# Kernel tuning notes

Hardware: AMD Instinct MI355X
Metric: run time of the kernel (lower is better)

The kernel has to match this reference:

```python
import jax, jax.numpy as jnp
import numpy as np

N_HEAD = 16
D_MODEL = 1024
D_K = 64
D_V = 64
TEMPER = float(np.power(D_MODEL, 0.5))  # NOTE: source scales by sqrt(d_model), not sqrt(d_k)


def setup_inputs() -> dict:
    key = jax.random.key(0)
    ks = jax.random.split(key, 6)
    B, T = 4, 2048
    q = jax.random.normal(ks[0], (B, T, D_MODEL), dtype=jnp.float32)
    k = jax.random.normal(ks[1], (B, T, D_MODEL), dtype=jnp.float32)
    v = jax.random.normal(ks[2], (B, T, D_MODEL), dtype=jnp.float32)
    # xavier_normal for [out, in] = [n_head*d, d_model]; stored as [d_model, n_head*d] for x @ W
    def xavier(kk, fan_out, fan_in):
        std = float(np.sqrt(2.0 / (fan_in + fan_out)))
        return jax.random.normal(kk, (fan_in, fan_out), dtype=jnp.float32) * std
    W_Q = xavier(ks[3], N_HEAD * D_K, D_MODEL)
    W_K = xavier(ks[4], N_HEAD * D_K, D_MODEL)
    W_V = xavier(ks[5], N_HEAD * D_V, D_MODEL)
    return {"q": q, "k": k, "v": v, "W_Q": W_Q, "W_K": W_K, "W_V": W_V}


def reference(q, k, v, W_Q, W_K, W_V):
    B, Tq, _ = q.shape
    Tk = k.shape[1]
    residual = q
    # project and split heads: [B, T, H, d]
    qh = (q @ W_Q).reshape(B, Tq, N_HEAD, D_K)
    kh = (k @ W_K).reshape(B, Tk, N_HEAD, D_K)
    vh = (v @ W_V).reshape(B, Tk, N_HEAD, D_V)
    # scaled dot-product attention (dropout is identity in eval)
    attn = jnp.einsum('bqhd,bkhd->bhqk', qh, kh) / TEMPER
    attn = jax.nn.softmax(attn, axis=-1)
    out = jnp.einsum('bhqk,bkhd->bqhd', attn, vh).reshape(B, Tq, N_HEAD * D_V)
    return out + residual
```

## Files before the change

kernel.cpp:

```cpp
#include <hip/hip_runtime.h>
#include <cstdint>
#include <cstddef>

typedef __bf16 bf16x8 __attribute__((ext_vector_type(8)));
typedef float f32x4 __attribute__((ext_vector_type(4)));
typedef unsigned short u16;
typedef unsigned int u32;

static constexpr int T = 2048;
static constexpr int DM = 1024;
static constexpr float QSCALE = 0.04508422f;

#define GLOBAL_AS __attribute__((address_space(1)))
#define LDS_AS __attribute__((address_space(3)))

__device__ __forceinline__ void gld_lds16(const u16* g, u16* l) {
  __builtin_amdgcn_global_load_lds((const GLOBAL_AS u32*)g, (LDS_AS u32*)l, 16, 0, 0);
}

__device__ __forceinline__ u16 f2bf(float f) {
  u32 u = __builtin_bit_cast(u32, f);
  u += 0x7fffu + ((u >> 16) & 1u);
  return (u16)(u >> 16);
}

__device__ __forceinline__ u32 pkb(float lo, float hi) {
#if __has_builtin(__builtin_amdgcn_cvt_pk_bf16_f32)
  typedef __bf16 bf16x2 __attribute__((ext_vector_type(2)));
  bf16x2 r = __builtin_amdgcn_cvt_pk_bf16_f32(lo, hi);
  return __builtin_bit_cast(u32, r);
#else
  return __builtin_amdgcn_perm(__builtin_bit_cast(u32, hi),
                               __builtin_bit_cast(u32, lo), 0x07060302u);
#endif
}

__device__ __forceinline__ float fexp2(float x) {
#if __has_builtin(__builtin_amdgcn_exp2f)
  return __builtin_amdgcn_exp2f(x);
#else
  return __builtin_exp2f(x);
#endif
}

__device__ __forceinline__ void pl16swap(u32& a, u32& b) {
  asm("v_permlane16_swap_b32 %0, %1" : "+v"(a), "+v"(b));
}
__device__ __forceinline__ void pl32swap(u32& a, u32& b) {
  asm("v_permlane32_swap_b32 %0, %1" : "+v"(a), "+v"(b));
}

__global__ __launch_bounds__(256) void xcvt(
    const float* __restrict__ q, const float* __restrict__ k, const float* __restrict__ v,
    u16* __restrict__ oq, u16* __restrict__ ok, u16* __restrict__ ov) {
  const float* X = blockIdx.y == 0 ? q : blockIdx.y == 1 ? k : v;
  u16* O = blockIdx.y == 0 ? oq : blockIdx.y == 1 ? ok : ov;
  const size_t i = ((size_t)blockIdx.x * 256 + threadIdx.x) * 8;
  float4 a0 = *(const float4*)(X + i), a1 = *(const float4*)(X + i + 4);
  uint4 p;
  p.x = pkb(a0.x, a0.y); p.y = pkb(a0.z, a0.w);
  p.z = pkb(a1.x, a1.y); p.w = pkb(a1.z, a1.w);
  *(uint4*)(O + i) = p;
}

__global__ __launch_bounds__(256) void wt_kernel(
    const float* __restrict__ W0, const float* __restrict__ W1, const float* __restrict__ W2,
    u16* __restrict__ O0, u16* __restrict__ O1, u16* __restrict__ O2) {
  const float* W = blockIdx.z == 0 ? W0 : blockIdx.z == 1 ? W1 : W2;
  u16* O = blockIdx.z == 0 ? O0 : blockIdx.z == 1 ? O1 : O2;
  const float sc = blockIdx.z == 0 ? QSCALE : 1.0f;
  const int k0 = blockIdx.x * 64, n0 = blockIdx.y * 64;
  __shared__ float tile[64][68];
  const int tid = threadIdx.x;
#pragma unroll
  for (int it = 0; it < 4; ++it) {
    int chunk = tid + it * 256;
    int r = chunk >> 4, c4 = (chunk & 15) * 4;
    *(float4*)&tile[r][c4] = *(const float4*)(W + (size_t)(k0 + r) * DM + n0 + c4);
  }
  __syncthreads();
#pragma unroll
  for (int it = 0; it < 4; ++it) {
    int chunk = tid + it * 256;
    int n = chunk >> 4, k4 = (chunk & 15) * 4;
    ushort4 o;
    o.x = f2bf(tile[k4 + 0][n] * sc);
    o.y = f2bf(tile[k4 + 1][n] * sc);
    o.z = f2bf(tile[k4 + 2][n] * sc);
    o.w = f2bf(tile[k4 + 3][n] * sc);
    *(ushort4*)(O + (size_t)(n0 + n) * DM + k0 + k4) = o;
  }
}

__global__ __launch_bounds__(256, 3) void gemm_proj(
    const u16* __restrict__ Xq, const u16* __restrict__ Xk, const u16* __restrict__ Xv,
    const u16* __restrict__ Wq, const u16* __restrict__ Wk, const u16* __restrict__ Wv,
    u16* __restrict__ Oq, u16* __restrict__ Ok, u16* __restrict__ VHt) {
  const int z = blockIdx.y;
  const u16* X = z == 0 ? Xq : z == 1 ? Xk : Xv;
  const u16* Wt = z == 0 ? Wq : z == 1 ? Wk : Wv;
  const int xcd = blockIdx.x & 7, j = blockIdx.x >> 3;
  const int n0 = (j & 7) * 128;
  const int m0 = (xcd * 8 + (j >> 3)) * 128;
  __shared__ u16 Al[128][64];
  __shared__ u16 Bl[128][64];
  const int tid = threadIdx.x, w = tid >> 6, lane = tid & 63;
  const int c16 = lane & 15, quad = lane >> 4;
  const int wm = (w >> 1) * 64, wn = (w & 1) * 64;
  const int rk = lane >> 3;
  const int ck = ((lane & 7) ^ rk) * 8;
  const int swz = c16 & 7;
  f32x4 acc[4][4] = {};
  const u16* ga = X + (size_t)(m0 + w * 32 + rk) * DM + ck;
  const u16* gb = Wt + (size_t)(n0 + w * 32 + rk) * DM + ck;
  for (int kk = 0; kk < 1024; kk += 64) {
    __syncthreads();
#pragma unroll
    for (int i = 0; i < 4; ++i) {
      gld_lds16(ga + kk + (size_t)(i * 8) * DM, &Al[w * 32 + i * 8][0]);
      gld_lds16(gb + kk + (size_t)(i * 8) * DM, &Bl[w * 32 + i * 8][0]);
    }
    __syncthreads();
#pragma unroll
    for (int s = 0; s < 2; ++s) {
      bf16x8 af[4], bfr[4];
#pragma unroll
      for (int t = 0; t < 4; ++t) af[t] = *(const bf16x8*)&Al[wm + t * 16 + c16][((quad + 4 * s) ^ swz) * 8];
#pragma unroll
      for (int t = 0; t < 4; ++t) bfr[t] = *(const bf16x8*)&Bl[wn + t * 16 + c16][((quad + 4 * s) ^ swz) * 8];
#pragma unroll
      for (int mt = 0; mt < 4; ++mt)
#pragma unroll
        for (int nt = 0; nt < 4; ++nt)
          acc[mt][nt] = __builtin_amdgcn_mfma_f32_16x16x32_bf16(af[mt], bfr[nt], acc[mt][nt], 0, 0, 0);
    }
  }
  if (z < 2) {
    u16* O = z == 0 ? Oq : Ok;
#pragma unroll
    for (int mt = 0; mt < 4; ++mt)
#pragma unroll
      for (int nt = 0; nt < 4; ++nt)
#pragma unroll
        for (int r = 0; r < 4; ++r) {
          size_t row = m0 + wm + mt * 16 + quad * 4 + r;
          size_t col = n0 + wn + nt * 16 + c16;
          O[row * DM + col] = f2bf(acc[mt][nt][r]);
        }
  } else {
#pragma unroll
    for (int mt = 0; mt < 4; ++mt)
#pragma unroll
      for (int nt = 0; nt < 4; ++nt) {
        const int row0 = m0 + wm + mt * 16 + quad * 4;
        const int col = n0 + wn + nt * 16 + c16;
        const int bb = row0 >> 11, t0 = row0 & 2047;
        const int hh = col >> 6, dd = col & 63;
        ushort4 o;
        o.x = f2bf(acc[mt][nt][0]);
        o.y = f2bf(acc[mt][nt][1]);
        o.z = f2bf(acc[mt][nt][2]);
        o.w = f2bf(acc[mt][nt][3]);
        *(ushort4*)(VHt + ((size_t)((bb * 16 + hh) * 64 + dd)) * T + t0) = o;
      }
  }
}

__global__ __launch_bounds__(256, 4) void flash_kernel(
    const u16* __restrict__ QH, const u16* __restrict__ KH, const u16* __restrict__ VHt,
    const float* __restrict__ res, float* __restrict__ out) {
  const int blk = blockIdx.x;
  const int x = blk & 7, g = blk >> 3;
  const int bh = x * 8 + (g & 7);
  const int qb = g >> 3;
  const int b = bh >> 4, h = bh & 15;
  const int tid = threadIdx.x, w = tid >> 6, lane = tid & 63;
  const int c16 = lane & 15, quad = lane >> 4;
  const int swzq = c16 & 7;
  __shared__ u16 Kl[2][64][64];
  __shared__ u16 Vt[2][64][64];
  __shared__ float Ll[4][2][16];
  const int qbase = qb * 128 + w * 32;
  bf16x8 bq[2][2];
#pragma unroll
  for (int qi = 0; qi < 2; ++qi) {
    const u16* qp = QH + (size_t)(b * T + qbase + qi * 16 + c16) * DM + h * 64 + quad * 8;
    bq[qi][0] = *(const bf16x8*)qp;
    bq[qi][1] = *(const bf16x8*)(qp + 32);
  }
  f32x4 acc[2][4] = {};
  float rs[2] = {0.f, 0.f};
  const int rk = lane >> 3;
  const int ck8 = ((lane & 7) ^ rk) * 8;
  const u16* kg = KH + (size_t)(b * T) * DM + h * 64 + ck8;
  const u16* vg = VHt + ((size_t)bh * 64 + w * 16 + rk) * T + ck8;
  {
    const u16* kg0 = kg + (size_t)(w * 16 + rk) * DM;
    gld_lds16(kg0, &Kl[0][w * 16][0]);
    gld_lds16(kg0 + (size_t)8 * DM, &Kl[0][w * 16 + 8][0]);
    gld_lds16(vg, &Vt[0][w * 16][0]);
    gld_lds16(vg + 8 * T, &Vt[0][w * 16 + 8][0]);
  }
  int cur = 0;
  for (int kt = 0; kt < 32; ++kt) {
    __builtin_amdgcn_s_barrier();
    if (kt < 31) {
      const u16* kg0 = kg + (size_t)((kt + 1) * 64 + w * 16 + rk) * DM;
      gld_lds16(kg0, &Kl[cur ^ 1][w * 16][0]);
      gld_lds16(kg0 + (size_t)8 * DM, &Kl[cur ^ 1][w * 16 + 8][0]);
      const u16* vg0 = vg + (kt + 1) * 64;
      gld_lds16(vg0, &Vt[cur ^ 1][w * 16][0]);
      gld_lds16(vg0 + (size_t)8 * T, &Vt[cur ^ 1][w * 16 + 8][0]);
      asm volatile("s_waitcnt vmcnt(4)" ::: "memory");
    } else {
      asm volatile("s_waitcnt vmcnt(0)" ::: "memory");
    }
    __builtin_amdgcn_s_barrier();
    bf16x8 ap[2][2];
    {
      bf16x8 ak[4][2];
#pragma unroll
      for (int mt = 0; mt < 4; ++mt) {
        const int r = mt * 16 + c16;
        ak[mt][0] = *(const bf16x8*)&Kl[cur][r][(quad ^ swzq) * 8];
        ak[mt][1] = *(const bf16x8*)&Kl[cur][r][((4 + quad) ^ swzq) * 8];
      }
#pragma unroll
      for (int qi = 0; qi < 2; ++qi) {
        u32 d[2][2][2];
#pragma unroll
        for (int mt = 0; mt < 4; ++mt) {
          f32x4 st = {};
          st = __builtin_amdgcn_mfma_f32_16x16x32_bf16(ak[mt][0], bq[qi][0], st, 0, 0, 0);
          st = __builtin_amdgcn_mfma_f32_16x16x32_bf16(ak[mt][1], bq[qi][1], st, 0, 0, 0);
          const float p0 = fexp2(st[0]), p1 = fexp2(st[1]);
          const float p2 = fexp2(st[2]), p3 = fexp2(st[3]);
          rs[qi] += (p0 + p1) + (p2 + p3);
          d[mt >> 1][mt & 1][0] = pkb(p0, p1);
          d[mt >> 1][mt & 1][1] = pkb(p2, p3);
        }
        pl32swap(d[0][0][0], d[0][1][0]);
        pl32swap(d[0][0][1], d[0][1][1]);
        pl32swap(d[1][0][0], d[1][1][0]);
        pl32swap(d[1][0][1], d[1][1][1]);
        pl16swap(d[0][0][0], d[0][1][0]);
        pl16swap(d[0][0][1], d[0][1][1]);
        pl16swap(d[1][0][0], d[1][1][0]);
        pl16swap(d[1][0][1], d[1][1][1]);
        uint4 a0 = {d[0][0][0], d[0][0][1], d[0][1][0], d[0][1][1]};
        uint4 a1 = {d[1][0][0], d[1][0][1], d[1][1][0], d[1][1][1]};
        ap[qi][0] = __builtin_bit_cast(bf16x8, a0);
        ap[qi][1] = __builtin_bit_cast(bf16x8, a1);
      }
    }
#pragma unroll
    for (int nt = 0; nt < 4; ++nt) {
      const int r = nt * 16 + c16;
      const bf16x8 bv0 = *(const bf16x8*)&Vt[cur][r][(quad ^ swzq) * 8];
      const bf16x8 bv1 = *(const bf16x8*)&Vt[cur][r][((4 + quad) ^ swzq) * 8];
#pragma unroll
      for (int qi = 0; qi < 2; ++qi) {
        acc[qi][nt] = __builtin_amdgcn_mfma_f32_16x16x32_bf16(ap[qi][0], bv0, acc[qi][nt], 0, 0, 0);
        acc[qi][nt] = __builtin_amdgcn_mfma_f32_16x16x32_bf16(ap[qi][1], bv1, acc[qi][nt], 0, 0, 0);
      }
    }
    cur ^= 1;
  }
#pragma unroll
  for (int qi = 0; qi < 2; ++qi) {
    float t = rs[qi];
    t += __shfl_xor(t, 16, 64);
    t += __shfl_xor(t, 32, 64);
    if (quad == 0) Ll[w][qi][c16] = t;
  }
  asm volatile("s_waitcnt lgkmcnt(0)" ::: "memory");
#pragma unroll
  for (int qi = 0; qi < 2; ++qi) {
    const f32x4 lv = *(const f32x4*)&Ll[w][qi][quad * 4];
#pragma unroll
    for (int r = 0; r < 4; ++r) {
      const float inv = 1.0f / lv[r];
      const size_t rowbase = (size_t)(b * T + qbase + qi * 16 + quad * 4 + r) * DM + h * 64;
#pragma unroll
      for (int nt = 0; nt < 4; ++nt) {
        const size_t idx = rowbase + nt * 16 + c16;
        out[idx] = acc[qi][nt][r] * inv + res[idx];
      }
    }
  }
}

extern "C" void kernel_launch(void* const* d_in, const int* in_sizes, int n_in,
                              void* d_out, int out_size, void* d_ws, size_t ws_size,
                              hipStream_t stream) {
  const float* q = (const float*)d_in[0];
  const float* k = (const float*)d_in[1];
  const float* v = (const float*)d_in[2];
  const float* WQ = (const float*)d_in[3];
  const float* WK = (const float*)d_in[4];
  const float* WV = (const float*)d_in[5];
  char* ws = (char*)d_ws;
  const size_t PH = (size_t)8192 * 1024 * 2;
  const size_t WT = (size_t)1024 * 1024 * 2;
  u16* XqB = (u16*)d_out;
  u16* XkB = (u16*)d_out + (size_t)8192 * 1024;
  u16* XvB = (u16*)(ws);
  u16* WtQ = (u16*)(ws + PH);
  u16* WtK = (u16*)(ws + PH + WT);
  u16* WtV = (u16*)(ws + PH + 2 * WT);
  u16* QH  = (u16*)(ws + PH + 3 * WT);
  u16* KH  = (u16*)(ws + 2 * PH + 3 * WT);
  u16* VHt = (u16*)(ws + 3 * PH + 3 * WT);

  xcvt<<<dim3(4096, 3), 256, 0, stream>>>(q, k, v, XqB, XkB, XvB);
  wt_kernel<<<dim3(16, 16, 3), 256, 0, stream>>>(WQ, WK, WV, WtQ, WtK, WtV);
  gemm_proj<<<dim3(512, 3), 256, 0, stream>>>(XqB, XkB, XvB, WtQ, WtK, WtV, QH, KH, VHt);
  flash_kernel<<<1024, 256, 0, stream>>>(QH, KH, VHt, q, (float*)d_out);
}
```

Before: 279.2 us.

## Replace projection GEMM with 256x256-tile, 8-wave double-buffered pipelined kernel

Rewrites the QKV projection GEMM to use 256x256 output tiles with 512 threads and 128KB of dynamic LDS. A/B tiles are double-buffered and the next K-slice is prefetched while MFMAs run, with barriers interleaving fragment loads and compute in four quadrant phases. Blocks are remapped across XCDs with a single flat grid. It also adds s_setprio around MFMA groups in both the GEMM and the flash kernel. The intent is more data reuse per LDS load and better overlap of memory with compute, at the cost of higher register pressure (128 accumulators per thread) and lower occupancy.

```diff
diff --git a/kernel.cpp b/kernel.cpp
--- a/kernel.cpp
+++ b/kernel.cpp
@@ -92,75 +92,154 @@
   }
 }
 
-__global__ __launch_bounds__(256, 3) void gemm_proj(
+__global__ __launch_bounds__(512, 2) void gemm8(
     const u16* __restrict__ Xq, const u16* __restrict__ Xk, const u16* __restrict__ Xv,
     const u16* __restrict__ Wq, const u16* __restrict__ Wk, const u16* __restrict__ Wv,
     u16* __restrict__ Oq, u16* __restrict__ Ok, u16* __restrict__ VHt) {
-  const int z = blockIdx.y;
+  extern __shared__ u16 lds[];
+  const int blk0 = blockIdx.x;
+  const int swz = (blk0 & 7) * 48 + (blk0 >> 3);
+  const int z = swz >> 7;
+  const int rr = swz & 127;
+  const int n0 = (rr & 3) * 256;
+  const int m0 = (rr >> 2) * 256;
   const u16* X = z == 0 ? Xq : z == 1 ? Xk : Xv;
-  const u16* Wt = z == 0 ? Wq : z == 1 ? Wk : Wv;
-  const int xcd = blockIdx.x & 7, j = blockIdx.x >> 3;
-  const int n0 = (j & 7) * 128;
-  const int m0 = (xcd * 8 + (j >> 3)) * 128;
-  __shared__ u16 Al[128][64];
-  __shared__ u16 Bl[128][64];
+  const u16* W = z == 0 ? Wq : z == 1 ? Wk : Wv;
   const int tid = threadIdx.x, w = tid >> 6, lane = tid & 63;
   const int c16 = lane & 15, quad = lane >> 4;
-  const int wm = (w >> 1) * 64, wn = (w & 1) * 64;
+  const int wm2 = w >> 2, wn4 = w & 3;
   const int rk = lane >> 3;
   const int ck = ((lane & 7) ^ rk) * 8;
-  const int swz = c16 & 7;
-  f32x4 acc[4][4] = {};
-  const u16* ga = X + (size_t)(m0 + w * 32 + rk) * DM + ck;
-  const u16* gb = Wt + (size_t)(n0 + w * 32 + rk) * DM + ck;
-  for (int kk = 0; kk < 1024; kk += 64) {
-    __syncthreads();
-#pragma unroll
-    for (int i = 0; i < 4; ++i) {
-      gld_lds16(ga + kk + (size_t)(i * 8) * DM, &Al[w * 32 + i * 8][0]);
-      gld_lds16(gb + kk + (size_t)(i * 8) * DM, &Bl[w * 32 + i * 8][0]);
-    }
-    __syncthreads();
-#pragma unroll
-    for (int s = 0; s < 2; ++s) {
-      bf16x8 af[4], bfr[4];
-#pragma unroll
-      for (int t = 0; t < 4; ++t) af[t] = *(const bf16x8*)&Al[wm + t * 16 + c16][((quad + 4 * s) ^ swz) * 8];
-#pragma unroll
-      for (int t = 0; t < 4; ++t) bfr[t] = *(const bf16x8*)&Bl[wn + t * 16 + c16][((quad + 4 * s) ^ swz) * 8];
-#pragma unroll
-      for (int mt = 0; mt < 4; ++mt)
-#pragma unroll
-        for (int nt = 0; nt < 4; ++nt)
-          acc[mt][nt] = __builtin_amdgcn_mfma_f32_16x16x32_bf16(af[mt], bfr[nt], acc[mt][nt], 0, 0, 0);
-    }
+  const int swzr = c16 & 7;
+  u16* As = lds;
+  u16* Bs = lds + 2 * 256 * 64;
+  f32x4 acc[8][4] = {};
+  const u16* gA = X + (size_t)(m0 + w * 8 + rk) * DM + ck;
+  const u16* gB = W + (size_t)(n0 + w * 8 + rk) * DM + ck;
+#pragma unroll
+  for (int u = 0; u < 4; ++u)
+    gld_lds16(gA + (size_t)(u * 64) * DM, As + (u * 64 + w * 8) * 64);
+#pragma unroll
+  for (int u = 0; u < 4; ++u)
+    gld_lds16(gB + (size_t)(u * 64) * DM, Bs + (u * 64 + w * 8) * 64);
+
+  bf16x8 af[4][2], bfA[2][2], bfB[2][2];
+  for (int kt = 0; kt < 16; ++kt) {
+    const int p = kt & 1, tn = kt + 1;
+    const u16* Ab = As + p * 16384;
+    const u16* Bb = Bs + p * 16384;
+    u16* An = As + (p ^ 1) * 16384;
+    u16* Bn = Bs + (p ^ 1) * 16384;
+    if (tn < 16) {
+      const size_t ko = (size_t)tn * 64;
+#pragma unroll
+      for (int u = 0; u < 4; ++u)
+        gld_lds16(gA + (size_t)(u * 64) * DM + ko, An + (u * 64 + w * 8) * 64);
+      asm volatile("s_waitcnt vmcnt(4)" ::: "memory");
+    } else {
+      asm volatile("s_waitcnt vmcnt(0)" ::: "memory");
+    }
+    __builtin_amdgcn_s_barrier();
+#pragma unroll
+    for (int f = 0; f < 4; ++f) {
+      const int R = wm2 * 128 + f * 16 + c16;
+      af[f][0] = *(const bf16x8*)&Ab[R * 64 + ((quad    ) ^ swzr) * 8];
+      af[f][1] = *(const bf16x8*)&Ab[R * 64 + ((quad + 4) ^ swzr) * 8];
+    }
+#pragma unroll
+    for (int g = 0; g < 2; ++g) {
+      const int R = wn4 * 64 + g * 16 + c16;
+      bfA[g][0] = *(const bf16x8*)&Bb[R * 64 + ((quad    ) ^ swzr) * 8];
+      bfA[g][1] = *(const bf16x8*)&Bb[R * 64 + ((quad + 4) ^ swzr) * 8];
+    }
+    __builtin_amdgcn_s_setprio(1);
+#pragma unroll
+    for (int f = 0; f < 4; ++f)
+#pragma unroll
+      for (int g = 0; g < 2; ++g) {
+        acc[f][g] = __builtin_amdgcn_mfma_f32_16x16x32_bf16(af[f][0], bfA[g][0], acc[f][g], 0, 0, 0);
+        acc[f][g] = __builtin_amdgcn_mfma_f32_16x16x32_bf16(af[f][1], bfA[g][1], acc[f][g], 0, 0, 0);
+      }
+    __builtin_amdgcn_s_setprio(0);
+    __builtin_amdgcn_s_barrier();
+#pragma unroll
+    for (int g = 0; g < 2; ++g) {
+      const int R = wn4 * 64 + 32 + g * 16 + c16;
+      bfB[g][0] = *(const bf16x8*)&Bb[R * 64 + ((quad    ) ^ swzr) * 8];
+      bfB[g][1] = *(const bf16x8*)&Bb[R * 64 + ((quad + 4) ^ swzr) * 8];
+    }
+    if (tn < 16) {
+      const size_t ko = (size_t)tn * 64;
+#pragma unroll
+      for (int u = 0; u < 4; ++u)
+        gld_lds16(gB + (size_t)(u * 64) * DM + ko, Bn + (u * 64 + w * 8) * 64);
+    }
+    __builtin_amdgcn_s_barrier();
+    __builtin_amdgcn_s_setprio(1);
+#pragma unroll
+    for (int f = 0; f < 4; ++f)
+#pragma unroll
+      for (int g = 0; g < 2; ++g) {
+        acc[f][2 + g] = __builtin_amdgcn_mfma_f32_16x16x32_bf16(af[f][0], bfB[g][0], acc[f][2 + g], 0, 0, 0);
+        acc[f][2 + g] = __builtin_amdgcn_mfma_f32_16x16x32_bf16(af[f][1], bfB[g][1], acc[f][2 + g], 0, 0, 0);
+      }
+    __builtin_amdgcn_s_setprio(0);
+    __builtin_amdgcn_s_barrier();
+#pragma unroll
+    for (int f = 0; f < 4; ++f) {
+      const int R = wm2 * 128 + 64 + f * 16 + c16;
+      af[f][0] = *(const bf16x8*)&Ab[R * 64 + ((quad    ) ^ swzr) * 8];
+      af[f][1] = *(const bf16x8*)&Ab[R * 64 + ((quad + 4) ^ swzr) * 8];
+    }
+    __builtin_amdgcn_s_barrier();
+    __builtin_amdgcn_s_setprio(1);
+#pragma unroll
+    for (int f = 0; f < 4; ++f)
+#pragma unroll
+      for (int g = 0; g < 2; ++g) {
+        acc[4 + f][2 + g] = __builtin_amdgcn_mfma_f32_16x16x32_bf16(af[f][0], bfB[g][0], acc[4 + f][2 + g], 0, 0, 0);
+        acc[4 + f][2 + g] = __builtin_amdgcn_mfma_f32_16x16x32_bf16(af[f][1], bfB[g][1], acc[4 + f][2 + g], 0, 0, 0);
+      }
+    __builtin_amdgcn_s_setprio(0);
+    __builtin_amdgcn_s_barrier();
+    __builtin_amdgcn_s_barrier();
+    __builtin_amdgcn_s_setprio(1);
+#pragma unroll
+    for (int f = 0; f < 4; ++f)
+#pragma unroll
+      for (int g = 0; g < 2; ++g) {
+        acc[4 + f][g] = __builtin_amdgcn_mfma_f32_16x16x32_bf16(af[f][0], bfA[g][0], acc[4 + f][g], 0, 0, 0);
+        acc[4 + f][g] = __builtin_amdgcn_mfma_f32_16x16x32_bf16(af[f][1], bfA[g][1], acc[4 + f][g], 0, 0, 0);
+      }
+    __builtin_amdgcn_s_setprio(0);
+    __builtin_amdgcn_s_barrier();
   }
   if (z < 2) {
     u16* O = z == 0 ? Oq : Ok;
 #pragma unroll
-    for (int mt = 0; mt < 4; ++mt)
-#pragma unroll
-      for (int nt = 0; nt < 4; ++nt)
+    for (int i = 0; i < 8; ++i)
+#pragma unroll
+      for (int j = 0; j < 4; ++j)
 #pragma unroll
         for (int r = 0; r < 4; ++r) {
-          size_t row = m0 + wm + mt * 16 + quad * 4 + r;
-          size_t col = n0 + wn + nt * 16 + c16;
-          O[row * DM + col] = f2bf(acc[mt][nt][r]);
+          size_t row = m0 + wm2 * 128 + i * 16 + quad * 4 + r;
+          size_t col = n0 + wn4 * 64 + j * 16 + c16;
+          O[row * DM + col] = f2bf(acc[i][j][r]);
         }
   } else {
 #pragma unroll
-    for (int mt = 0; mt < 4; ++mt)
-#pragma unroll
-      for (int nt = 0; nt < 4; ++nt) {
-        const int row0 = m0 + wm + mt * 16 + quad * 4;
-        const int col = n0 + wn + nt * 16 + c16;
+    for (int i = 0; i < 8; ++i)
+#pragma unroll
+      for (int j = 0; j < 4; ++j) {
+        const int row0 = m0 + wm2 * 128 + i * 16 + quad * 4;
+        const int col = n0 + wn4 * 64 + j * 16 + c16;
         const int bb = row0 >> 11, t0 = row0 & 2047;
         const int hh = col >> 6, dd = col & 63;
         ushort4 o;
-        o.x = f2bf(acc[mt][nt][0]);
-        o.y = f2bf(acc[mt][nt][1]);
-        o.z = f2bf(acc[mt][nt][2]);
-        o.w = f2bf(acc[mt][nt][3]);
+        o.x = f2bf(acc[i][j][0]);
+        o.y = f2bf(acc[i][j][1]);
+        o.z = f2bf(acc[i][j][2]);
+        o.w = f2bf(acc[i][j][3]);
         *(ushort4*)(VHt + ((size_t)((bb * 16 + hh) * 64 + dd)) * T + t0) = o;
       }
   }
@@ -231,8 +310,10 @@
 #pragma unroll
         for (int mt = 0; mt < 4; ++mt) {
           f32x4 st = {};
+          __builtin_amdgcn_s_setprio(1);
           st = __builtin_amdgcn_mfma_f32_16x16x32_bf16(ak[mt][0], bq[qi][0], st, 0, 0, 0);
           st = __builtin_amdgcn_mfma_f32_16x16x32_bf16(ak[mt][1], bq[qi][1], st, 0, 0, 0);
+          __builtin_amdgcn_s_setprio(0);
           const float p0 = fexp2(st[0]), p1 = fexp2(st[1]);
           const float p2 = fexp2(st[2]), p3 = fexp2(st[3]);
           rs[qi] += (p0 + p1) + (p2 + p3);
@@ -258,11 +339,13 @@
       const int r = nt * 16 + c16;
       const bf16x8 bv0 = *(const bf16x8*)&Vt[cur][r][(quad ^ swzq) * 8];
       const bf16x8 bv1 = *(const bf16x8*)&Vt[cur][r][((4 + quad) ^ swzq) * 8];
+      __builtin_amdgcn_s_setprio(1);
 #pragma unroll
       for (int qi = 0; qi < 2; ++qi) {
         acc[qi][nt] = __builtin_amdgcn_mfma_f32_16x16x32_bf16(ap[qi][0], bv0, acc[qi][nt], 0, 0, 0);
         acc[qi][nt] = __builtin_amdgcn_mfma_f32_16x16x32_bf16(ap[qi][1], bv1, acc[qi][nt], 0, 0, 0);
       }
+      __builtin_amdgcn_s_setprio(0);
     }
     cur ^= 1;
   }
@@ -312,8 +395,11 @@
   u16* KH  = (u16*)(ws + 2 * PH + 3 * WT);
   u16* VHt = (u16*)(ws + 3 * PH + 3 * WT);
 
+  hipFuncSetAttribute(reinterpret_cast<const void*>(gemm8),
+                      hipFuncAttributeMaxDynamicSharedMemorySize, 131072);
+
   xcvt<<<dim3(4096, 3), 256, 0, stream>>>(q, k, v, XqB, XkB, XvB);
   wt_kernel<<<dim3(16, 16, 3), 256, 0, stream>>>(WQ, WK, WV, WtQ, WtK, WtV);
-  gemm_proj<<<dim3(512, 3), 256, 0, stream>>>(XqB, XkB, XvB, WtQ, WtK, WtV, QH, KH, VHt);
+  gemm8<<<dim3(384), 512, 131072, stream>>>(XqB, XkB, XvB, WtQ, WtK, WtV, QH, KH, VHt);
   flash_kernel<<<1024, 256, 0, stream>>>(QH, KH, VHt, q, (float*)d_out);
 }
```

Result: slower. 348.4 us (+24.8%).

## Rewrite projection GEMM with double-buffered LDS, 128x256 tiles and XCD-affine mapping

Applied to the files above, without the earlier changes.

Replaces the projection GEMM with a 512-thread kernel using 128x256 tiles, a K-step of 32, and double-buffered LDS. The next tile's global-to-LDS loads are issued before the current tile's MFMAs, so load latency overlaps compute. Blocks are mapped so each XCD works on a contiguous region of M and N, which should improve L2 reuse. s_setprio is also wrapped around MFMA bursts in both the GEMM and the flash kernel. The cost is a new swizzle scheme and more barriers per K step.

```diff
diff --git a/kernel.cpp b/kernel.cpp
--- a/kernel.cpp
+++ b/kernel.cpp
@@ -92,75 +92,94 @@
   }
 }
 
-__global__ __launch_bounds__(256, 3) void gemm_proj(
+__global__ __launch_bounds__(512, 2) void gemm_aff(
     const u16* __restrict__ Xq, const u16* __restrict__ Xk, const u16* __restrict__ Xv,
     const u16* __restrict__ Wq, const u16* __restrict__ Wk, const u16* __restrict__ Wv,
     u16* __restrict__ Oq, u16* __restrict__ Ok, u16* __restrict__ VHt) {
-  const int z = blockIdx.y;
+  __shared__ u16 As[2][64][64];
+  __shared__ u16 Bs[2][128][64];
+  const int blk = blockIdx.x;
+  const int xcd = blk & 7, j = blk >> 3;
+  const int z = j >> 5;
+  const int rem = j & 31;
+  const int m0 = (xcd >> 1) * 2048 + (rem >> 1) * 128;
+  const int n0 = (xcd & 1) * 512 + (rem & 1) * 256;
   const u16* X = z == 0 ? Xq : z == 1 ? Xk : Xv;
-  const u16* Wt = z == 0 ? Wq : z == 1 ? Wk : Wv;
-  const int xcd = blockIdx.x & 7, j = blockIdx.x >> 3;
-  const int n0 = (j & 7) * 128;
-  const int m0 = (xcd * 8 + (j >> 3)) * 128;
-  __shared__ u16 Al[128][64];
-  __shared__ u16 Bl[128][64];
+  const u16* W = z == 0 ? Wq : z == 1 ? Wk : Wv;
   const int tid = threadIdx.x, w = tid >> 6, lane = tid & 63;
   const int c16 = lane & 15, quad = lane >> 4;
-  const int wm = (w >> 1) * 64, wn = (w & 1) * 64;
-  const int rk = lane >> 3;
-  const int ck = ((lane & 7) ^ rk) * 8;
-  const int swz = c16 & 7;
+  const int wm = w >> 2, wn = w & 3;
+  const int rk = lane >> 3, cc = lane & 7, L = cc ^ rk;
+  const int rowo = 2 * rk + (L >> 2), ko = (L & 3) * 8;
+  const u16* gA = X + (size_t)(m0 + 16 * w + rowo) * DM + ko;
+  const u16* gB0 = W + (size_t)(n0 + 32 * w + rowo) * DM + ko;
+  const u16* gB1 = gB0 + (size_t)16 * DM;
+  u16* lA = &As[0][w * 8][0];
+  u16* lB0 = &Bs[0][w * 16][0];
+  u16* lB1 = &Bs[0][w * 16 + 8][0];
+  const int ccr = ((c16 & 1) * 4 + quad) ^ (c16 >> 1);
+  const int offA = (32 * wm + (c16 >> 1)) * 64 + ccr * 8;
+  const int offB = (32 * wn + (c16 >> 1)) * 64 + ccr * 8;
   f32x4 acc[4][4] = {};
-  const u16* ga = X + (size_t)(m0 + w * 32 + rk) * DM + ck;
-  const u16* gb = Wt + (size_t)(n0 + w * 32 + rk) * DM + ck;
-  for (int kk = 0; kk < 1024; kk += 64) {
-    __syncthreads();
-#pragma unroll
-    for (int i = 0; i < 4; ++i) {
-      gld_lds16(ga + kk + (size_t)(i * 8) * DM, &Al[w * 32 + i * 8][0]);
-      gld_lds16(gb + kk + (size_t)(i * 8) * DM, &Bl[w * 32 + i * 8][0]);
-    }
-    __syncthreads();
-#pragma unroll
-    for (int s = 0; s < 2; ++s) {
-      bf16x8 af[4], bfr[4];
-#pragma unroll
-      for (int t = 0; t < 4; ++t) af[t] = *(const bf16x8*)&Al[wm + t * 16 + c16][((quad + 4 * s) ^ swz) * 8];
-#pragma unroll
-      for (int t = 0; t < 4; ++t) bfr[t] = *(const bf16x8*)&Bl[wn + t * 16 + c16][((quad + 4 * s) ^ swz) * 8];
-#pragma unroll
-      for (int mt = 0; mt < 4; ++mt)
-#pragma unroll
-        for (int nt = 0; nt < 4; ++nt)
-          acc[mt][nt] = __builtin_amdgcn_mfma_f32_16x16x32_bf16(af[mt], bfr[nt], acc[mt][nt], 0, 0, 0);
-    }
+  gld_lds16(gA, lA);
+  gld_lds16(gB0, lB0);
+  gld_lds16(gB1, lB1);
+#pragma unroll 2
+  for (int kt = 0; kt < 32; ++kt) {
+    const int buf = kt & 1;
+    __builtin_amdgcn_s_barrier();
+    if (kt < 31) {
+      const size_t go = (size_t)(kt + 1) * 32;
+      const int nA = (buf ^ 1) * 4096, nB = (buf ^ 1) * 8192;
+      gld_lds16(gA + go, lA + nA);
+      gld_lds16(gB0 + go, lB0 + nB);
+      gld_lds16(gB1 + go, lB1 + nB);
+      asm volatile("s_waitcnt vmcnt(3)" ::: "memory");
+    } else {
+      asm volatile("s_waitcnt vmcnt(0)" ::: "memory");
+    }
+    __builtin_amdgcn_s_barrier();
+    const u16* Ab = &As[buf][0][0];
+    const u16* Bb = &Bs[buf][0][0];
+    bf16x8 af[4], bf[4];
+#pragma unroll
+    for (int f = 0; f < 4; ++f) af[f] = *(const bf16x8*)(Ab + offA + f * 512);
+#pragma unroll
+    for (int n = 0; n < 4; ++n) bf[n] = *(const bf16x8*)(Bb + offB + n * 512);
+    __builtin_amdgcn_s_setprio(1);
+#pragma unroll
+    for (int f = 0; f < 4; ++f)
+#pragma unroll
+      for (int n = 0; n < 4; ++n)
+        acc[f][n] = __builtin_amdgcn_mfma_f32_16x16x32_bf16(af[f], bf[n], acc[f][n], 0, 0, 0);
+    __builtin_amdgcn_s_setprio(0);
   }
   if (z < 2) {
     u16* O = z == 0 ? Oq : Ok;
 #pragma unroll
-    for (int mt = 0; mt < 4; ++mt)
-#pragma unroll
-      for (int nt = 0; nt < 4; ++nt)
+    for (int f = 0; f < 4; ++f)
+#pragma unroll
+      for (int n = 0; n < 4; ++n)
 #pragma unroll
         for (int r = 0; r < 4; ++r) {
-          size_t row = m0 + wm + mt * 16 + quad * 4 + r;
-          size_t col = n0 + wn + nt * 16 + c16;
-          O[row * DM + col] = f2bf(acc[mt][nt][r]);
+          size_t row = m0 + wm * 64 + f * 16 + quad * 4 + r;
+          size_t col = n0 + wn * 64 + n * 16 + c16;
+          O[row * DM + col] = f2bf(acc[f][n][r]);
         }
   } else {
 #pragma unroll
-    for (int mt = 0; mt < 4; ++mt)
-#pragma unroll
-      for (int nt = 0; nt < 4; ++nt) {
-        const int row0 = m0 + wm + mt * 16 + quad * 4;
-        const int col = n0 + wn + nt * 16 + c16;
+    for (int f = 0; f < 4; ++f)
+#pragma unroll
+      for (int n = 0; n < 4; ++n) {
+        const int row0 = m0 + wm * 64 + f * 16 + quad * 4;
+        const int col = n0 + wn * 64 + n * 16 + c16;
         const int bb = row0 >> 11, t0 = row0 & 2047;
         const int hh = col >> 6, dd = col & 63;
         ushort4 o;
-        o.x = f2bf(acc[mt][nt][0]);
-        o.y = f2bf(acc[mt][nt][1]);
-        o.z = f2bf(acc[mt][nt][2]);
-        o.w = f2bf(acc[mt][nt][3]);
+        o.x = f2bf(acc[f][n][0]);
+        o.y = f2bf(acc[f][n][1]);
+        o.z = f2bf(acc[f][n][2]);
+        o.w = f2bf(acc[f][n][3]);
         *(ushort4*)(VHt + ((size_t)((bb * 16 + hh) * 64 + dd)) * T + t0) = o;
       }
   }
@@ -231,8 +250,10 @@
 #pragma unroll
         for (int mt = 0; mt < 4; ++mt) {
           f32x4 st = {};
+          __builtin_amdgcn_s_setprio(1);
           st = __builtin_amdgcn_mfma_f32_16x16x32_bf16(ak[mt][0], bq[qi][0], st, 0, 0, 0);
           st = __builtin_amdgcn_mfma_f32_16x16x32_bf16(ak[mt][1], bq[qi][1], st, 0, 0, 0);
+          __builtin_amdgcn_s_setprio(0);
           const float p0 = fexp2(st[0]), p1 = fexp2(st[1]);
           const float p2 = fexp2(st[2]), p3 = fexp2(st[3]);
           rs[qi] += (p0 + p1) + (p2 + p3);
@@ -258,11 +279,13 @@
       const int r = nt * 16 + c16;
       const bf16x8 bv0 = *(const bf16x8*)&Vt[cur][r][(quad ^ swzq) * 8];
       const bf16x8 bv1 = *(const bf16x8*)&Vt[cur][r][((4 + quad) ^ swzq) * 8];
+      __builtin_amdgcn_s_setprio(1);
 #pragma unroll
       for (int qi = 0; qi < 2; ++qi) {
         acc[qi][nt] = __builtin_amdgcn_mfma_f32_16x16x32_bf16(ap[qi][0], bv0, acc[qi][nt], 0, 0, 0);
         acc[qi][nt] = __builtin_amdgcn_mfma_f32_16x16x32_bf16(ap[qi][1], bv1, acc[qi][nt], 0, 0, 0);
       }
+      __builtin_amdgcn_s_setprio(0);
     }
     cur ^= 1;
   }
@@ -314,6 +337,6 @@
 
   xcvt<<<dim3(4096, 3), 256, 0, stream>>>(q, k, v, XqB, XkB, XvB);
   wt_kernel<<<dim3(16, 16, 3), 256, 0, stream>>>(WQ, WK, WV, WtQ, WtK, WtV);
-  gemm_proj<<<dim3(512, 3), 256, 0, stream>>>(XqB, XkB, XvB, WtQ, WtK, WtV, QH, KH, VHt);
+  gemm_aff<<<dim3(768), 512, 0, stream>>>(XqB, XkB, XvB, WtQ, WtK, WtV, QH, KH, VHt);
   flash_kernel<<<1024, 256, 0, stream>>>(QH, KH, VHt, q, (float*)d_out);
 }
```

New measurement: 362.1 us. 1.3x slower.
